# Performance work log

Measured on AMD Instinct MI355X. Metric: run time of the kernel, lower is better.

The kernel has to match this reference:

```python
import jax, jax.numpy as jnp
import numpy as np

B, C_IN, H, W = 4, 128, 32, 128   # W must equal out_channels (fc_out acts on last dim)
C_OUT, NUM_HEADS = 128, 2
BN_EPS = 1e-5


def setup_inputs() -> dict:
    key = jax.random.key(0)
    ks = jax.random.split(key, 14)
    s = 0.05  # small init scale for weights
    d = {
        "x": jax.random.normal(ks[0], (B, C_IN, H, W), jnp.float32),
        "wq": jax.random.normal(ks[1], (C_OUT, C_IN), jnp.float32) * s,
        "bq": jax.random.normal(ks[2], (C_OUT,), jnp.float32) * s,
        "wk": jax.random.normal(ks[3], (C_OUT, C_IN), jnp.float32) * s,
        "bk": jax.random.normal(ks[4], (C_OUT,), jnp.float32) * s,
        "wv": jax.random.normal(ks[5], (C_OUT, C_IN), jnp.float32) * s,
        "bv": jax.random.normal(ks[6], (C_OUT,), jnp.float32) * s,
        "fc_w": jax.random.normal(ks[7], (C_OUT, C_OUT), jnp.float32) * s,
        "fc_b": jax.random.normal(ks[8], (C_OUT,), jnp.float32) * s,
        "bn_gamma": jnp.ones((C_OUT,), jnp.float32),
        "bn_beta": jnp.zeros((C_OUT,), jnp.float32),
        "bn_mean": jax.random.normal(ks[9], (C_OUT,), jnp.float32) * 0.1,
        "bn_var": jax.random.uniform(ks[10], (C_OUT,), jnp.float32, 0.5, 1.5),
        "prelu_a": jnp.full((1,), 0.25, jnp.float32),
    }
    return d


def reference(x, wq, bq, wk, bk, wv, bv, fc_w, fc_b,
              bn_gamma, bn_beta, bn_mean, bn_var, prelu_a):
    b, c_in, h, w = x.shape
    c_out = wq.shape[0]
    nh = NUM_HEADS
    dk = c_out // nh
    L = h * w
    xf = x.reshape(b, c_in, L)                                # (B, Cin, L)
    # 1x1 convs == per-token linear projections
    q = jnp.einsum('oi,bil->bol', wq, xf) + bq[:, None]       # (B, Cout, L)
    k = jnp.einsum('oi,bil->bol', wk, xf) + bk[:, None]
    v = jnp.einsum('oi,bil->bol', wv, xf) + bv[:, None]
    Q = q.reshape(b, nh, dk, L)                               # (B, h, d_k, L)
    K = k.reshape(b, nh, dk, L)
    V = v.reshape(b, nh, dk, L)
    # scaled dot-product attention over the L = H*W tokens
    scores = jnp.einsum('bhdl,bhdm->bhlm', Q, K) / jnp.sqrt(jnp.float32(dk))
    attn = jax.nn.softmax(scores, axis=-1)                    # (B, h, L, L)
    out = jnp.einsum('bhlm,bhdm->bhdl', attn, V)              # (B, h, d_k, L)
    out = out.reshape(b, c_out, h, w)                         # (B, Cout, H, W)
    # fc_out: torch Linear on the LAST dim (W == Cout)
    y = jnp.einsum('bchw,ow->bcho', out, fc_w) + fc_b         # (B, Cout, H, W)
    # BatchNorm2d (eval mode: running stats) over channel dim
    inv = jax.lax.rsqrt(bn_var + BN_EPS)
    y = (y - bn_mean[None, :, None, None]) * (inv * bn_gamma)[None, :, None, None] \
        + bn_beta[None, :, None, None]
    # PReLU (single shared slope); dropout is identity in eval
    y = jnp.where(y > 0, y, prelu_a[0] * y)
    return y
```

## Files before the change

kernel.cpp:

```cpp
#include <hip/hip_runtime.h>

typedef _Float16 f16x8 __attribute__((ext_vector_type(8)));
typedef _Float16 f16x4t __attribute__((ext_vector_type(4)));
typedef __fp16 h16x2 __attribute__((ext_vector_type(2)));
typedef float f32x4 __attribute__((ext_vector_type(4)));
typedef float f32x16 __attribute__((ext_vector_type(16)));

#define L_SZ 4096

__device__ __forceinline__ unsigned short f2h(float f) {
    _Float16 h = (_Float16)f;
    return __builtin_bit_cast(unsigned short, h);
}
__device__ __forceinline__ unsigned int pk2(float a, float b) {
    h16x2 p = __builtin_amdgcn_cvt_pkrtz(a, b);
    return __builtin_bit_cast(unsigned int, p);
}

#define SLOT(row, ci) ((((ci) * 64) + ((row) & 32) + (((row) & 31) ^ (ci))) * 8)

__global__ __launch_bounds__(256, 1) void qkv_kernel(
    const float* __restrict__ x,
    const float* __restrict__ wq, const float* __restrict__ bq,
    const float* __restrict__ wk, const float* __restrict__ bk,
    const float* __restrict__ wv, const float* __restrict__ bv,
    unsigned short* __restrict__ Qp, unsigned short* __restrict__ Kp,
    unsigned short* __restrict__ Vp)
{
    int blk = blockIdx.x;
    int bidx = blk >> 6;
    int l0 = (blk & 63) * 64;
    int tid = threadIdx.x;
    int wave = tid >> 6, lane = tid & 63;
    int c = lane & 15, qd = lane >> 4;

    __shared__ __align__(16) unsigned short Ws[384 * 128];
    __shared__ __align__(16) unsigned short Sc[9216];

    #pragma unroll
    for (int t = 0; t < 96; ++t) {
        int e2 = tid + t * 256;
        const float* src = (e2 < 8192) ? wq : (e2 < 16384 ? wk : wv);
        int eo = (e2 * 2) & 16383;
        float2 v = *(const float2*)&src[eo];
        int e = e2 * 2;
        int o = e >> 7, ci = (e & 127) >> 3, j = e & 7;
        *(unsigned int*)&Ws[o * 128 + ((ci ^ (o & 15)) * 8) + j] = pk2(v.x, v.y);
    }

    unsigned short* Xs = Sc;
    #pragma unroll
    for (int it = 0; it < 8; ++it) {
        int i  = (tid >> 4) + 16 * it;
        int l4 = (tid & 15) * 4;
        const float4 v = *(const float4*)&x[(bidx * 128 + i) * L_SZ + l0 + l4];
        float vv[4] = {v.x, v.y, v.z, v.w};
        int ci = i >> 3;
        #pragma unroll
        for (int u = 0; u < 4; ++u) {
            int l = l4 + u;
            Xs[l * 128 + ((ci ^ (l & 15)) * 8) + (i & 7)] = f2h(vv[u]);
        }
    }
    __syncthreads();

    f16x8 afrag[4];
    #pragma unroll
    for (int kc = 0; kc < 4; ++kc) {
        int l = wave * 16 + c;
        int ci = kc * 4 + qd;
        afrag[kc] = *(const f16x8*)&Xs[l * 128 + ((ci ^ (l & 15)) * 8)];
    }
    __syncthreads();

    f32x4 acc[24];
    #pragma unroll
    for (int nt = 0; nt < 24; ++nt) acc[nt] = (f32x4){0.f, 0.f, 0.f, 0.f};

    #pragma unroll
    for (int kc = 0; kc < 4; ++kc) {
        #pragma unroll
        for (int nt = 0; nt < 24; ++nt) {
            int o = nt * 16 + c;
            f16x8 bfrag = *(const f16x8*)&Ws[o * 128 + (((kc * 4 + qd) ^ c) * 8)];
            acc[nt] = __builtin_amdgcn_mfma_f32_16x16x32_f16(afrag[kc], bfrag, acc[nt], 0, 0, 0);
        }
    }

    unsigned short* Vt = Sc;
    const float s_q = 0.18033688011f;
    #pragma unroll
    for (int nt = 0; nt < 24; ++nt) {
        int p = nt >> 3;
        int o = (nt & 7) * 16 + c;
        int h = o >> 6, d = o & 63;
        #pragma unroll
        for (int r = 0; r < 4; ++r) {
            int ll = wave * 16 + qd * 4 + r;
            int l = l0 + ll;
            float val = acc[nt][r];
            if (p == 0) {
                val = (val + bq[o]) * s_q;
                Qp[((bidx * 2 + h) * L_SZ + l) * 64 + d] = f2h(val);
            } else if (p == 1) {
                val += bk[o];
                Kp[((bidx * 2 + h) * L_SZ + l) * 64 + d] = f2h(val);
            } else {
                val += bv[o];
                Vt[o * 72 + ll] = f2h(val);
            }
        }
    }
    __syncthreads();
    #pragma unroll
    for (int t = 0; t < 2; ++t) {
        int u = tid + t * 256;
        int row = u >> 2;
        int lc = (u & 3) * 16;
        uint4 a0 = *(const uint4*)&Vt[row * 72 + lc];
        uint4 a1 = *(const uint4*)&Vt[row * 72 + lc + 8];
        *(uint4*)&Vp[(size_t)(bidx * 128 + row) * L_SZ + l0 + lc] = a0;
        *(uint4*)&Vp[(size_t)(bidx * 128 + row) * L_SZ + l0 + lc + 8] = a1;
    }
}

__global__ __launch_bounds__(256, 3) void attn_kernel(
    const unsigned short* __restrict__ Qp, const unsigned short* __restrict__ Kp,
    const unsigned short* __restrict__ Vp,
    unsigned short* __restrict__ Opart, float* __restrict__ Mpart, float* __restrict__ Lpart)
{
    int blk = blockIdx.x;
    int lt = blk & 31;
    int bh = (blk >> 5) & 7;
    int sp = blk >> 8;
    int l0 = lt * 128;
    int tid = threadIdx.x;
    int wave = tid >> 6, lane = tid & 63;
    int ln = lane & 31, hi = lane >> 5;
    int b = bh >> 1, h = bh & 1;

    __shared__ __align__(16) unsigned short Ks[2][4096];
    __shared__ __align__(16) unsigned short Vs[2][4096];
    __shared__ __align__(16) unsigned short Ps[4][2048];

    const unsigned short* Qb = Qp + (size_t)bh * L_SZ * 64;
    const unsigned short* Kb = Kp + (size_t)bh * L_SZ * 64;
    const unsigned short* Vb = Vp + ((size_t)b * 128 + h * 64) * L_SZ;

    int lq = l0 + wave * 32 + ln;
    f16x8 qf[4];
    #pragma unroll
    for (int kc = 0; kc < 4; ++kc)
        qf[kc] = *(const f16x8*)&Qb[(size_t)lq * 64 + kc * 16 + hi * 8];

    float m_st = -1e30f, lsum = 0.f;
    f32x16 acc0 = {}, acc1 = {};

    int urow = tid >> 3, uci = tid & 7;
    int mglob = sp * 1024;

    uint4 kreg[2], vreg[2];
    #pragma unroll
    for (int j = 0; j < 2; ++j) {
        int row = urow + j * 32;
        kreg[j] = *(const uint4*)&Kb[(size_t)(mglob + row) * 64 + uci * 8];
        vreg[j] = *(const uint4*)&Vb[(size_t)row * L_SZ + mglob + uci * 8];
    }
    #pragma unroll
    for (int j = 0; j < 2; ++j) {
        int row = urow + j * 32;
        *(uint4*)&Ks[0][SLOT(row, uci)] = kreg[j];
        *(uint4*)&Vs[0][SLOT(row, uci)] = vreg[j];
    }

    for (int it = 0; it < 16; ++it) {
        int cur = it & 1;
        __syncthreads();
        if (it < 15) {
            int m0 = mglob + (it + 1) * 64;
            #pragma unroll
            for (int j = 0; j < 2; ++j) {
                int row = urow + j * 32;
                kreg[j] = *(const uint4*)&Kb[(size_t)(m0 + row) * 64 + uci * 8];
                vreg[j] = *(const uint4*)&Vb[(size_t)row * L_SZ + m0 + uci * 8];
            }
        }

        f32x16 s0 = {}, s1 = {};
        #pragma unroll
        for (int kc = 0; kc < 4; ++kc) {
            int cd = kc * 2 + hi;
            f16x8 k0 = *(const f16x8*)&Ks[cur][SLOT(ln, cd)];
            f16x8 k1 = *(const f16x8*)&Ks[cur][SLOT(32 + ln, cd)];
            s0 = __builtin_amdgcn_mfma_f32_32x32x16_f16(k0, qf[kc], s0, 0, 0, 0);
            s1 = __builtin_amdgcn_mfma_f32_32x32x16_f16(k1, qf[kc], s1, 0, 0, 0);
        }

        float mx = s0[0];
        #pragma unroll
        for (int r = 1; r < 16; ++r) mx = fmaxf(mx, s0[r]);
        #pragma unroll
        for (int r = 0; r < 16; ++r) mx = fmaxf(mx, s1[r]);
        mx = fmaxf(mx, __shfl_xor(mx, 32));
        float mnew = fmaxf(m_st, mx);
        float alpha = exp2f(m_st - mnew);
        m_st = mnew;
        float rsum = 0.f;
        #pragma unroll
        for (int r = 0; r < 16; ++r) { float p = exp2f(s0[r] - mnew); s0[r] = p; rsum += p; }
        #pragma unroll
        for (int r = 0; r < 16; ++r) { float p = exp2f(s1[r] - mnew); s1[r] = p; rsum += p; }
        lsum = lsum * alpha + rsum;
        #pragma unroll
        for (int r = 0; r < 16; ++r) { acc0[r] *= alpha; acc1[r] *= alpha; }

        #pragma unroll
        for (int g = 0; g < 4; ++g) {
            uint2 w0;
            w0.x = pk2(s0[g * 4 + 0], s0[g * 4 + 1]);
            w0.y = pk2(s0[g * 4 + 2], s0[g * 4 + 3]);
            *(uint2*)&Ps[wave][(g * 32 + (ln ^ g)) * 8 + hi * 4] = w0;
            int g2 = 4 + g;
            uint2 w1;
            w1.x = pk2(s1[g * 4 + 0], s1[g * 4 + 1]);
            w1.y = pk2(s1[g * 4 + 2], s1[g * 4 + 3]);
            *(uint2*)&Ps[wave][(g2 * 32 + (ln ^ g2)) * 8 + hi * 4] = w1;
        }

        #pragma unroll
        for (int kc = 0; kc < 4; ++kc) {
            int cd = kc * 2 + hi;
            f16x8 pf = *(const f16x8*)&Ps[wave][(cd * 32 + (ln ^ cd)) * 8];
            f16x8 v0 = *(const f16x8*)&Vs[cur][SLOT(ln, cd)];
            f16x8 v1 = *(const f16x8*)&Vs[cur][SLOT(32 + ln, cd)];
            acc0 = __builtin_amdgcn_mfma_f32_32x32x16_f16(v0, pf, acc0, 0, 0, 0);
            acc1 = __builtin_amdgcn_mfma_f32_32x32x16_f16(v1, pf, acc1, 0, 0, 0);
        }

        if (it < 15) {
            #pragma unroll
            for (int j = 0; j < 2; ++j) {
                int row = urow + j * 32;
                *(uint4*)&Ks[cur ^ 1][SLOT(row, uci)] = kreg[j];
                *(uint4*)&Vs[cur ^ 1][SLOT(row, uci)] = vreg[j];
            }
        }
    }

    float l_tot = lsum + __shfl_xor(lsum, 32);
    unsigned short* Ow = Opart + (size_t)(sp * 8 + bh) * 64 * 4096;
    #pragma unroll
    for (int r = 0; r < 16; ++r) {
        int d0 = (r & 3) + 8 * (r >> 2) + 4 * hi;
        Ow[(size_t)d0 * 4096 + lq] = f2h(acc0[r]);
        Ow[(size_t)(32 + d0) * 4096 + lq] = f2h(acc1[r]);
    }
    if (hi == 0) {
        Mpart[(sp * 8 + bh) * 4096 + lq] = m_st;
        Lpart[(sp * 8 + bh) * 4096 + lq] = l_tot;
    }
}

__global__ __launch_bounds__(256, 1) void fc_kernel(
    const unsigned short* __restrict__ Opart, const float* __restrict__ Mp,
    const float* __restrict__ Lp, const float* __restrict__ fcw_f,
    const float* __restrict__ fc_b, const float* __restrict__ bn_g,
    const float* __restrict__ bn_b, const float* __restrict__ bn_m,
    const float* __restrict__ bn_v, const float* __restrict__ prelu_a,
    float* __restrict__ out)
{
    int blk = blockIdx.x;
    int r0 = blk * 64;
    int tid = threadIdx.x;
    int c0 = (r0 >> 5) & 127;
    int bh = (r0 >> 12) * 2 + (c0 >> 6);

    __shared__ __align__(16) unsigned short Fw[128 * 128];
    __shared__ __align__(16) unsigned short SclU[4096 * 4];

    #pragma unroll
    for (int t = 0; t < 16; ++t) {
        int l = tid + t * 256;
        float m0 = Mp[(0 * 8 + bh) * 4096 + l], m1 = Mp[(1 * 8 + bh) * 4096 + l];
        float m2 = Mp[(2 * 8 + bh) * 4096 + l], m3 = Mp[(3 * 8 + bh) * 4096 + l];
        float mx = fmaxf(fmaxf(m0, m1), fmaxf(m2, m3));
        float a0 = exp2f(m0 - mx), a1 = exp2f(m1 - mx);
        float a2 = exp2f(m2 - mx), a3 = exp2f(m3 - mx);
        float den = a0 * Lp[(0 * 8 + bh) * 4096 + l] + a1 * Lp[(1 * 8 + bh) * 4096 + l]
                  + a2 * Lp[(2 * 8 + bh) * 4096 + l] + a3 * Lp[(3 * 8 + bh) * 4096 + l];
        float inv = 1.0f / den;
        int hh = l >> 7, ww = l & 127;
        int slot = hh * 128 + ((ww + hh) & 127);
        uint2 sc;
        sc.x = pk2(a0 * inv, a1 * inv);
        sc.y = pk2(a2 * inv, a3 * inv);
        *(uint2*)&SclU[slot * 4] = sc;
    }
    #pragma unroll
    for (int t = 0; t < 32; ++t) {
        int e2 = tid + t * 256;
        float2 v = *(const float2*)&fcw_f[e2 * 2];
        int e = e2 * 2;
        int o = e >> 7, ci = (e & 127) >> 3, j = e & 7;
        *(unsigned int*)&Fw[o * 128 + ((ci ^ (o & 15)) * 8) + j] = pk2(v.x, v.y);
    }
    __syncthreads();

    int wave = tid >> 6, lane = tid & 63;
    int c = lane & 15, qd = lane >> 4;
    int rw = r0 + wave * 16;
    int row = rw + c;
    int ch = (row >> 5) & 127, hh = row & 31, d = ch & 63;

    f16x8 af[4];
    #pragma unroll
    for (int kc = 0; kc < 4; ++kc) {
        int w0 = kc * 32 + qd * 8;
        f16x8 ov[4];
        #pragma unroll
        for (int s = 0; s < 4; ++s)
            ov[s] = *(const f16x8*)&Opart[(size_t)(s * 8 + bh) * 262144 + (size_t)d * 4096 + hh * 128 + w0];
        #pragma unroll
        for (int j = 0; j < 8; ++j) {
            int slot = hh * 128 + ((w0 + j + hh) & 127);
            f16x4t sc = *(const f16x4t*)&SclU[slot * 4];
            float v = (float)ov[0][j] * (float)sc[0] + (float)ov[1][j] * (float)sc[1]
                    + (float)ov[2][j] * (float)sc[2] + (float)ov[3][j] * (float)sc[3];
            af[kc][j] = (_Float16)v;
        }
    }

    f32x4 acc[8];
    #pragma unroll
    for (int nt = 0; nt < 8; ++nt) acc[nt] = (f32x4){0.f, 0.f, 0.f, 0.f};
    #pragma unroll
    for (int kc = 0; kc < 4; ++kc) {
        #pragma unroll
        for (int nt = 0; nt < 8; ++nt) {
            int o = nt * 16 + c;
            f16x8 bf = *(const f16x8*)&Fw[o * 128 + (((kc * 4 + qd) ^ c) * 8)];
            acc[nt] = __builtin_amdgcn_mfma_f32_16x16x32_f16(af[kc], bf, acc[nt], 0, 0, 0);
        }
    }

    float pa = prelu_a[0];
    #pragma unroll
    for (int r = 0; r < 4; ++r) {
        int orow = rw + qd * 4 + r;
        int chn = (orow >> 5) & 127;
        float g  = bn_g[chn] * rsqrtf(bn_v[chn] + 1e-5f);
        float mn = bn_m[chn], bt = bn_b[chn];
        #pragma unroll
        for (int nt = 0; nt < 8; ++nt) {
            int o = nt * 16 + c;
            float y = (acc[nt][r] + fc_b[o] - mn) * g + bt;
            y = y > 0.f ? y : pa * y;
            out[(size_t)orow * 128 + o] = y;
        }
    }
}

extern "C" void kernel_launch(void* const* d_in, const int* in_sizes, int n_in,
                              void* d_out, int out_size, void* d_ws, size_t ws_size,
                              hipStream_t stream) {
    const float* x     = (const float*)d_in[0];
    const float* wq    = (const float*)d_in[1];
    const float* bq    = (const float*)d_in[2];
    const float* wk    = (const float*)d_in[3];
    const float* bk    = (const float*)d_in[4];
    const float* wv    = (const float*)d_in[5];
    const float* bv    = (const float*)d_in[6];
    const float* fcw_f = (const float*)d_in[7];
    const float* fcb   = (const float*)d_in[8];
    const float* bn_g  = (const float*)d_in[9];
    const float* bn_b  = (const float*)d_in[10];
    const float* bn_m  = (const float*)d_in[11];
    const float* bn_v  = (const float*)d_in[12];
    const float* pa    = (const float*)d_in[13];
    float* out = (float*)d_out;

    unsigned short* Qp  = (unsigned short*)d_ws;
    unsigned short* Kp  = Qp + 8 * L_SZ * 64;
    unsigned short* Vp  = Kp + 8 * L_SZ * 64;
    unsigned short* Opart = Vp + 8 * L_SZ * 64;
    float* Mpart = (float*)(Opart + 4 * 8 * 64 * L_SZ);
    float* Lpart = Mpart + 4 * 8 * L_SZ;

    hipLaunchKernelGGL(qkv_kernel,  dim3(256),  dim3(256), 0, stream,
                       x, wq, bq, wk, bk, wv, bv, Qp, Kp, Vp);
    hipLaunchKernelGGL(attn_kernel, dim3(1024), dim3(256), 0, stream,
                       Qp, Kp, Vp, Opart, Mpart, Lpart);
    hipLaunchKernelGGL(fc_kernel,   dim3(256),  dim3(256), 0, stream,
                       Opart, Mpart, Lpart, fcw_f, fcb, bn_g, bn_b, bn_m, bn_v, pa, out);
}
```

Before: 169.7 us.

## Prepack weights once, register-shuffle P, lazy softmax rescale, remap blocks

Adds a prep kernel that converts the QKV and fc weights to swizzled fp16 images once per call, so the qkv and fc kernels copy them directly instead of each block converting fp32 weights. In attention, the P tile moves between lane halves with permlane32_swap instead of a round trip through shared memory, the max rescale is skipped when the new row max stays within a threshold of the running max, the max reduction becomes a tree, and wave priority is raised around the MFMA section. It also raises the occupancy hint to 4, remaps block indices for locality, and hoists the Opart loads in the fc kernel. This costs an extra kernel launch, and the lazy rescale relies on fp16 headroom for the unrescaled exponentials.

```diff
diff --git a/kernel.cpp b/kernel.cpp
--- a/kernel.cpp
+++ b/kernel.cpp
@@ -5,6 +5,7 @@
 typedef __fp16 h16x2 __attribute__((ext_vector_type(2)));
 typedef float f32x4 __attribute__((ext_vector_type(4)));
 typedef float f32x16 __attribute__((ext_vector_type(16)));
+typedef unsigned int uint2v __attribute__((ext_vector_type(2)));
 
 #define L_SZ 4096
 
@@ -19,11 +20,31 @@
 
 #define SLOT(row, ci) ((((ci) * 64) + ((row) & 32) + (((row) & 31) ^ (ci))) * 8)
 
+__global__ __launch_bounds__(256) void prep_kernel(
+    const float* __restrict__ wq, const float* __restrict__ wk,
+    const float* __restrict__ wv, const float* __restrict__ fcw,
+    unsigned short* __restrict__ Wimg, unsigned short* __restrict__ Fimg)
+{
+    int e2 = blockIdx.x * 256 + threadIdx.x;
+    if (e2 < 24576) {
+        const float* src = (e2 < 8192) ? wq : (e2 < 16384 ? wk : wv);
+        float2 v = *(const float2*)&src[(e2 * 2) & 16383];
+        int e = e2 * 2;
+        int o = e >> 7, ci = (e & 127) >> 3, j = e & 7;
+        *(unsigned int*)&Wimg[o * 128 + ((ci ^ (o & 15)) * 8) + j] = pk2(v.x, v.y);
+    } else {
+        int fe = (e2 - 24576) * 2;
+        float2 v = *(const float2*)&fcw[fe];
+        int o = fe >> 7, ci = (fe & 127) >> 3, j = fe & 7;
+        *(unsigned int*)&Fimg[o * 128 + ((ci ^ (o & 15)) * 8) + j] = pk2(v.x, v.y);
+    }
+}
+
 __global__ __launch_bounds__(256, 1) void qkv_kernel(
     const float* __restrict__ x,
-    const float* __restrict__ wq, const float* __restrict__ bq,
-    const float* __restrict__ wk, const float* __restrict__ bk,
-    const float* __restrict__ wv, const float* __restrict__ bv,
+    const unsigned short* __restrict__ Wimg,
+    const float* __restrict__ bq, const float* __restrict__ bk,
+    const float* __restrict__ bv,
     unsigned short* __restrict__ Qp, unsigned short* __restrict__ Kp,
     unsigned short* __restrict__ Vp)
 {
@@ -38,14 +59,9 @@
     __shared__ __align__(16) unsigned short Sc[9216];
 
     #pragma unroll
-    for (int t = 0; t < 96; ++t) {
-        int e2 = tid + t * 256;
-        const float* src = (e2 < 8192) ? wq : (e2 < 16384 ? wk : wv);
-        int eo = (e2 * 2) & 16383;
-        float2 v = *(const float2*)&src[eo];
-        int e = e2 * 2;
-        int o = e >> 7, ci = (e & 127) >> 3, j = e & 7;
-        *(unsigned int*)&Ws[o * 128 + ((ci ^ (o & 15)) * 8) + j] = pk2(v.x, v.y);
+    for (int t = 0; t < 24; ++t) {
+        int i8 = (tid + t * 256) * 8;
+        *(uint4*)&Ws[i8] = *(const uint4*)&Wimg[i8];
     }
 
     unsigned short* Xs = Sc;
@@ -124,12 +140,13 @@
     }
 }
 
-__global__ __launch_bounds__(256, 3) void attn_kernel(
+__global__ __launch_bounds__(256, 4) void attn_kernel(
     const unsigned short* __restrict__ Qp, const unsigned short* __restrict__ Kp,
     const unsigned short* __restrict__ Vp,
     unsigned short* __restrict__ Opart, float* __restrict__ Mpart, float* __restrict__ Lpart)
 {
-    int blk = blockIdx.x;
+    int raw = blockIdx.x;
+    int blk = (raw & 7) * 128 + (raw >> 3);
     int lt = blk & 31;
     int bh = (blk >> 5) & 7;
     int sp = blk >> 8;
@@ -141,7 +158,6 @@
 
     __shared__ __align__(16) unsigned short Ks[2][4096];
     __shared__ __align__(16) unsigned short Vs[2][4096];
-    __shared__ __align__(16) unsigned short Ps[4][2048];
 
     const unsigned short* Qb = Qp + (size_t)bh * L_SZ * 64;
     const unsigned short* Kb = Kp + (size_t)bh * L_SZ * 64;
@@ -186,6 +202,7 @@
             }
         }
 
+        __builtin_amdgcn_s_setprio(1);
         f32x16 s0 = {}, s1 = {};
         #pragma unroll
         for (int kc = 0; kc < 4; ++kc) {
@@ -196,46 +213,57 @@
             s1 = __builtin_amdgcn_mfma_f32_32x32x16_f16(k1, qf[kc], s1, 0, 0, 0);
         }
 
-        float mx = s0[0];
-        #pragma unroll
-        for (int r = 1; r < 16; ++r) mx = fmaxf(mx, s0[r]);
-        #pragma unroll
-        for (int r = 0; r < 16; ++r) mx = fmaxf(mx, s1[r]);
+        float t[8];
+        #pragma unroll
+        for (int r = 0; r < 8; ++r)
+            t[r] = fmaxf(fmaxf(s0[r], s0[r + 8]), fmaxf(s1[r], s1[r + 8]));
+        t[0] = fmaxf(t[0], t[4]); t[1] = fmaxf(t[1], t[5]);
+        t[2] = fmaxf(t[2], t[6]); t[3] = fmaxf(t[3], t[7]);
+        float mx = fmaxf(fmaxf(t[0], t[1]), fmaxf(t[2], t[3]));
         mx = fmaxf(mx, __shfl_xor(mx, 32));
-        float mnew = fmaxf(m_st, mx);
-        float alpha = exp2f(m_st - mnew);
-        m_st = mnew;
+
+        if (!__all(mx <= m_st + 8.0f)) {
+            float mnew = fmaxf(m_st, mx);
+            float alpha = exp2f(m_st - mnew);
+            m_st = mnew;
+            lsum *= alpha;
+            #pragma unroll
+            for (int r = 0; r < 16; ++r) { acc0[r] *= alpha; acc1[r] *= alpha; }
+        }
         float rsum = 0.f;
         #pragma unroll
-        for (int r = 0; r < 16; ++r) { float p = exp2f(s0[r] - mnew); s0[r] = p; rsum += p; }
-        #pragma unroll
-        for (int r = 0; r < 16; ++r) { float p = exp2f(s1[r] - mnew); s1[r] = p; rsum += p; }
-        lsum = lsum * alpha + rsum;
-        #pragma unroll
-        for (int r = 0; r < 16; ++r) { acc0[r] *= alpha; acc1[r] *= alpha; }
-
-        #pragma unroll
-        for (int g = 0; g < 4; ++g) {
-            uint2 w0;
-            w0.x = pk2(s0[g * 4 + 0], s0[g * 4 + 1]);
-            w0.y = pk2(s0[g * 4 + 2], s0[g * 4 + 3]);
-            *(uint2*)&Ps[wave][(g * 32 + (ln ^ g)) * 8 + hi * 4] = w0;
-            int g2 = 4 + g;
-            uint2 w1;
-            w1.x = pk2(s1[g * 4 + 0], s1[g * 4 + 1]);
-            w1.y = pk2(s1[g * 4 + 2], s1[g * 4 + 3]);
-            *(uint2*)&Ps[wave][(g2 * 32 + (ln ^ g2)) * 8 + hi * 4] = w1;
-        }
+        for (int r = 0; r < 16; ++r) { float p = exp2f(s0[r] - m_st); s0[r] = p; rsum += p; }
+        #pragma unroll
+        for (int r = 0; r < 16; ++r) { float p = exp2f(s1[r] - m_st); s1[r] = p; rsum += p; }
+        lsum += rsum;
 
         #pragma unroll
         for (int kc = 0; kc < 4; ++kc) {
+            unsigned int a0, a1, a2, a3;
+            if (kc == 0) {
+                a0 = pk2(s0[0], s0[1]);  a1 = pk2(s0[2], s0[3]);
+                a2 = pk2(s0[4], s0[5]);  a3 = pk2(s0[6], s0[7]);
+            } else if (kc == 1) {
+                a0 = pk2(s0[8], s0[9]);  a1 = pk2(s0[10], s0[11]);
+                a2 = pk2(s0[12], s0[13]); a3 = pk2(s0[14], s0[15]);
+            } else if (kc == 2) {
+                a0 = pk2(s1[0], s1[1]);  a1 = pk2(s1[2], s1[3]);
+                a2 = pk2(s1[4], s1[5]);  a3 = pk2(s1[6], s1[7]);
+            } else {
+                a0 = pk2(s1[8], s1[9]);  a1 = pk2(s1[10], s1[11]);
+                a2 = pk2(s1[12], s1[13]); a3 = pk2(s1[14], s1[15]);
+            }
+            uint2v r02 = __builtin_amdgcn_permlane32_swap(a0, a2, false, false);
+            uint2v r13 = __builtin_amdgcn_permlane32_swap(a1, a3, false, false);
+            uint4 pw; pw.x = r02[0]; pw.y = r13[0]; pw.z = r02[1]; pw.w = r13[1];
+            f16x8 pf = __builtin_bit_cast(f16x8, pw);
             int cd = kc * 2 + hi;
-            f16x8 pf = *(const f16x8*)&Ps[wave][(cd * 32 + (ln ^ cd)) * 8];
             f16x8 v0 = *(const f16x8*)&Vs[cur][SLOT(ln, cd)];
             f16x8 v1 = *(const f16x8*)&Vs[cur][SLOT(32 + ln, cd)];
             acc0 = __builtin_amdgcn_mfma_f32_32x32x16_f16(v0, pf, acc0, 0, 0, 0);
             acc1 = __builtin_amdgcn_mfma_f32_32x32x16_f16(v1, pf, acc1, 0, 0, 0);
         }
+        __builtin_amdgcn_s_setprio(0);
 
         if (it < 15) {
             #pragma unroll
@@ -263,20 +291,36 @@
 
 __global__ __launch_bounds__(256, 1) void fc_kernel(
     const unsigned short* __restrict__ Opart, const float* __restrict__ Mp,
-    const float* __restrict__ Lp, const float* __restrict__ fcw_f,
+    const float* __restrict__ Lp, const unsigned short* __restrict__ Fimg,
     const float* __restrict__ fc_b, const float* __restrict__ bn_g,
     const float* __restrict__ bn_b, const float* __restrict__ bn_m,
     const float* __restrict__ bn_v, const float* __restrict__ prelu_a,
     float* __restrict__ out)
 {
-    int blk = blockIdx.x;
+    int raw = blockIdx.x;
+    int blk = (raw & 7) * 32 + (raw >> 3);
     int r0 = blk * 64;
     int tid = threadIdx.x;
     int c0 = (r0 >> 5) & 127;
     int bh = (r0 >> 12) * 2 + (c0 >> 6);
 
+    int wave = tid >> 6, lane = tid & 63;
+    int c = lane & 15, qd = lane >> 4;
+    int rw = r0 + wave * 16;
+    int row = rw + c;
+    int ch = (row >> 5) & 127, hh = row & 31, d = ch & 63;
+
     __shared__ __align__(16) unsigned short Fw[128 * 128];
     __shared__ __align__(16) unsigned short SclU[4096 * 4];
+
+    uint4 ovr[4][4];
+    #pragma unroll
+    for (int kc = 0; kc < 4; ++kc) {
+        int w0 = kc * 32 + qd * 8;
+        #pragma unroll
+        for (int s = 0; s < 4; ++s)
+            ovr[kc][s] = *(const uint4*)&Opart[(size_t)(s * 8 + bh) * 262144 + (size_t)d * 4096 + hh * 128 + w0];
+    }
 
     #pragma unroll
     for (int t = 0; t < 16; ++t) {
@@ -289,43 +333,34 @@
         float den = a0 * Lp[(0 * 8 + bh) * 4096 + l] + a1 * Lp[(1 * 8 + bh) * 4096 + l]
                   + a2 * Lp[(2 * 8 + bh) * 4096 + l] + a3 * Lp[(3 * 8 + bh) * 4096 + l];
         float inv = 1.0f / den;
-        int hh = l >> 7, ww = l & 127;
-        int slot = hh * 128 + ((ww + hh) & 127);
+        int hl = l >> 7, ww = l & 127;
+        int slot = hl * 128 + ((ww + hl) & 127);
         uint2 sc;
         sc.x = pk2(a0 * inv, a1 * inv);
         sc.y = pk2(a2 * inv, a3 * inv);
         *(uint2*)&SclU[slot * 4] = sc;
     }
     #pragma unroll
-    for (int t = 0; t < 32; ++t) {
-        int e2 = tid + t * 256;
-        float2 v = *(const float2*)&fcw_f[e2 * 2];
-        int e = e2 * 2;
-        int o = e >> 7, ci = (e & 127) >> 3, j = e & 7;
-        *(unsigned int*)&Fw[o * 128 + ((ci ^ (o & 15)) * 8) + j] = pk2(v.x, v.y);
+    for (int t = 0; t < 8; ++t) {
+        int i8 = (tid + t * 256) * 8;
+        *(uint4*)&Fw[i8] = *(const uint4*)&Fimg[i8];
     }
     __syncthreads();
-
-    int wave = tid >> 6, lane = tid & 63;
-    int c = lane & 15, qd = lane >> 4;
-    int rw = r0 + wave * 16;
-    int row = rw + c;
-    int ch = (row >> 5) & 127, hh = row & 31, d = ch & 63;
 
     f16x8 af[4];
     #pragma unroll
     for (int kc = 0; kc < 4; ++kc) {
         int w0 = kc * 32 + qd * 8;
-        f16x8 ov[4];
-        #pragma unroll
-        for (int s = 0; s < 4; ++s)
-            ov[s] = *(const f16x8*)&Opart[(size_t)(s * 8 + bh) * 262144 + (size_t)d * 4096 + hh * 128 + w0];
+        f16x8 ov0 = __builtin_bit_cast(f16x8, ovr[kc][0]);
+        f16x8 ov1 = __builtin_bit_cast(f16x8, ovr[kc][1]);
+        f16x8 ov2 = __builtin_bit_cast(f16x8, ovr[kc][2]);
+        f16x8 ov3 = __builtin_bit_cast(f16x8, ovr[kc][3]);
         #pragma unroll
         for (int j = 0; j < 8; ++j) {
             int slot = hh * 128 + ((w0 + j + hh) & 127);
             f16x4t sc = *(const f16x4t*)&SclU[slot * 4];
-            float v = (float)ov[0][j] * (float)sc[0] + (float)ov[1][j] * (float)sc[1]
-                    + (float)ov[2][j] * (float)sc[2] + (float)ov[3][j] * (float)sc[3];
+            float v = (float)ov0[j] * (float)sc[0] + (float)ov1[j] * (float)sc[1]
+                    + (float)ov2[j] * (float)sc[2] + (float)ov3[j] * (float)sc[3];
             af[kc][j] = (_Float16)v;
         }
     }
@@ -385,11 +420,15 @@
     unsigned short* Opart = Vp + 8 * L_SZ * 64;
     float* Mpart = (float*)(Opart + 4 * 8 * 64 * L_SZ);
     float* Lpart = Mpart + 4 * 8 * L_SZ;
-
+    unsigned short* Wimg = (unsigned short*)(Lpart + 4 * 8 * L_SZ);
+    unsigned short* Fimg = Wimg + 384 * 128;
+
+    hipLaunchKernelGGL(prep_kernel, dim3(128),  dim3(256), 0, stream,
+                       wq, wk, wv, fcw_f, Wimg, Fimg);
     hipLaunchKernelGGL(qkv_kernel,  dim3(256),  dim3(256), 0, stream,
-                       x, wq, bq, wk, bk, wv, bv, Qp, Kp, Vp);
+                       x, Wimg, bq, bk, bv, Qp, Kp, Vp);
     hipLaunchKernelGGL(attn_kernel, dim3(1024), dim3(256), 0, stream,
                        Qp, Kp, Vp, Opart, Mpart, Lpart);
     hipLaunchKernelGGL(fc_kernel,   dim3(256),  dim3(256), 0, stream,
-                       Opart, Mpart, Lpart, fcw_f, fcb, bn_g, bn_b, bn_m, bn_v, pa, out);
-}
+                       Opart, Mpart, Lpart, Fimg, fcb, bn_g, bn_b, bn_m, bn_v, pa, out);
+}
```

Result: no change. 172.7 us (+1.8%).
